# Optimization experiments

Hardware: AMD Instinct MI355X
Metric: run time of the kernel (lower is better)

## Reference

```python
import jax, jax.numpy as jnp
import numpy as np

B, N, D = 16, 256, 32


def setup_inputs() -> dict:
    key = jax.random.key(0)
    ks = jax.random.split(key, 9)
    s = lambda fan_in: 1.0 / np.sqrt(fan_in)
    return {
        "x": jax.random.normal(ks[0], (B, N, D), dtype=jnp.float32),
        # fc_out: Linear(2D -> D), stored as [in, out]
        "W_out": jax.random.uniform(ks[1], (2 * D, D), minval=-s(2 * D), maxval=s(2 * D)),
        "b_out": jax.random.uniform(ks[2], (D,), minval=-s(2 * D), maxval=s(2 * D)),
        # fc_cat: Linear(D -> 1)
        "W_cat": jax.random.uniform(ks[3], (D, 1), minval=-s(D), maxval=s(D)),
        "b_cat": jax.random.uniform(ks[4], (1,), minval=-s(D), maxval=s(D)),
        # att_fusion: Linear(2->8), ReLU, Linear(8->1), Sigmoid
        "W_f1": jax.random.uniform(ks[5], (2, 8), minval=-s(2), maxval=s(2)),
        "b_f1": jax.random.uniform(ks[6], (8,), minval=-s(2), maxval=s(2)),
        "W_f2": jax.random.uniform(ks[7], (8, 1), minval=-s(8), maxval=s(8)),
        "b_f2": jax.random.uniform(ks[8], (1,), minval=-s(8), maxval=s(8)),
    }


def reference(x, W_out, b_out, W_cat, b_cat, W_f1, b_f1, W_f2, b_f2):
    b, n, d = x.shape
    # Edge (i,j): receiver = x[:, i], sender = x[:, j] (off-diagonal only).
    # Vectorized over all N*N pairs instead of one-hot matmuls + batch loop.
    senders = jnp.broadcast_to(x[:, None, :, :], (b, n, n, d))    # x[j] at (i,j)
    receivers = jnp.broadcast_to(x[:, :, None, :], (b, n, n, d))  # x[i] at (i,j)
    pair = jnp.concatenate([senders, receivers], axis=-1)         # [B,N,N,2D]
    h = jax.nn.relu(pair @ W_out + b_out)                         # [B,N,N,D]
    e = jax.nn.relu(h @ W_cat + b_cat)                            # [B,N,N,1]
    off_diag = (1.0 - jnp.eye(n, dtype=x.dtype))[None, :, :, None]
    m_lin = e * off_diag                                          # zeros on diagonal (scatter equivalent)
    m_prod = jnp.einsum('bid,bjd->bij', x, x)[..., None]          # [B,N,N,1]
    fused = jnp.concatenate([m_lin, m_prod], axis=-1)             # [B,N,N,2]
    w = jax.nn.sigmoid(jax.nn.relu(fused @ W_f1 + b_f1) @ W_f2 + b_f2)  # [B,N,N,1]
    m = w * m_lin + (1.0 - w) * m_prod
    m = m + jnp.mean(m, axis=-2, keepdims=True)
    # F.layer_norm over shape[1:] = (N,N,1), no affine
    mu = jnp.mean(m, axis=(1, 2, 3), keepdims=True)
    var = jnp.var(m, axis=(1, 2, 3), keepdims=True)
    return (m - mu) / jnp.sqrt(var + 1e-5)
```

## Files before the change

### kernel.cpp

```cpp
#include <hip/hip_runtime.h>
#include <math.h>

#define BB 16
#define NN 256
#define DD 32

__global__ __launch_bounds__(256) void uvT_kernel(
    const float* __restrict__ x,
    const float* __restrict__ W_out,
    const float* __restrict__ b_out,
    float* __restrict__ uT, float* __restrict__ xT, float* __restrict__ vT)
{
    __shared__ float lxA[256];
    int t = threadIdx.x;
    int g0 = blockIdx.x * 8;
    lxA[t] = x[(size_t)g0 * DD + t];
    __syncthreads();

    int nl = t >> 5, d = t & 31;
    int b  = (g0 + nl) >> 8;
    int n  = (g0 + nl) & 255;
    float su = 0.f, sv = 0.f;
#pragma unroll
    for (int k = 0; k < DD; ++k) {
        float xv = lxA[nl * DD + k];
        su += xv * W_out[k * DD + d];
        sv += xv * W_out[(k + DD) * DD + d];
    }
    int idxT = ((b * 8 + (d >> 2)) * NN + n) * 4 + (d & 3);
    uT[idxT] = su;
    vT[idxT] = sv + b_out[d];
    xT[idxT] = lxA[nl * DD + d];
}

__global__ __launch_bounds__(256) void pair_kernel(
    const float* __restrict__ uT, const float* __restrict__ xT,
    const float* __restrict__ vT,
    const float* __restrict__ W_cat, const float* __restrict__ b_cat,
    const float* __restrict__ W_f1,  const float* __restrict__ b_f1,
    const float* __restrict__ W_f2,  const float* __restrict__ b_f2,
    float* __restrict__ m_out,
    float* __restrict__ rowsum_out, float* __restrict__ rowsq_out)
{
    __shared__ float red0[8][4], red1[8][4];

    const int t  = threadIdx.x;
    const int b  = blockIdx.x >> 5;
    const int i0 = (blockIdx.x & 31) * 8;

    const float4* uT4 = (const float4*)uT;
    const float4* xT4 = (const float4*)xT;
    const float4* vT4 = (const float4*)vT;

    float4 uj[8], xj[8];
#pragma unroll
    for (int q = 0; q < 8; ++q) {
        uj[q] = uT4[(b * 8 + q) * NN + t];
        xj[q] = xT4[(b * 8 + q) * NN + t];
    }

    const float4* Wc4 = (const float4*)W_cat;
    float4 wc[8];
#pragma unroll
    for (int q = 0; q < 8; ++q) wc[q] = Wc4[q];
    float f1a[8], f1b[8], fb1[8], f2w[8];
#pragma unroll
    for (int k = 0; k < 8; ++k) {
        f1a[k] = W_f1[k];
        f1b[k] = W_f1[8 + k];
        fb1[k] = b_f1[k];
        f2w[k] = W_f2[k];
    }
    const float bcat = b_cat[0], bf2 = b_f2[0];

    const int lane = t & 63, wv = t >> 6;
    float mreg[8];
#pragma unroll
    for (int r = 0; r < 8; ++r) {
        int i = i0 + r;
        float e = 0.f, mp = 0.f;
#pragma unroll
        for (int q = 0; q < 8; ++q) {
            float4 vi = vT4[(b * 8 + q) * NN + i];
            float4 xi = xT4[(b * 8 + q) * NN + i];
            float4 uu = uj[q], xx = xj[q];
            e += fmaxf(uu.x + vi.x, 0.f) * wc[q].x;
            e += fmaxf(uu.y + vi.y, 0.f) * wc[q].y;
            e += fmaxf(uu.z + vi.z, 0.f) * wc[q].z;
            e += fmaxf(uu.w + vi.w, 0.f) * wc[q].w;
            mp += xx.x * xi.x + xx.y * xi.y + xx.z * xi.z + xx.w * xi.w;
        }
        e = fmaxf(e + bcat, 0.f);
        float mlin = (t == i) ? 0.f : e;
        float s = bf2;
#pragma unroll
        for (int k = 0; k < 8; ++k)
            s += fmaxf(mlin * f1a[k] + mp * f1b[k] + fb1[k], 0.f) * f2w[k];
        float w = 1.f / (1.f + expf(-s));
        float m = w * mlin + (1.f - w) * mp;
        mreg[r] = m;

        float sm = m, sq = m * m;
#pragma unroll
        for (int off = 32; off; off >>= 1) {
            sm += __shfl_down(sm, off);
            sq += __shfl_down(sq, off);
        }
        if (lane == 0) { red0[r][wv] = sm; red1[r][wv] = sq; }
    }

#pragma unroll
    for (int r = 0; r < 8; ++r)
        m_out[((size_t)b * NN + i0 + r) * NN + t] = mreg[r];

    __syncthreads();
    if (t < 8) {
        rowsum_out[b * NN + i0 + t] = red0[t][0] + red0[t][1] + red0[t][2] + red0[t][3];
        rowsq_out [b * NN + i0 + t] = red1[t][0] + red1[t][1] + red1[t][2] + red1[t][3];
    }
}

__global__ __launch_bounds__(256) void final_kernel(
    const float* __restrict__ m_in,
    const float* __restrict__ rowsum, const float* __restrict__ rowsq,
    float* __restrict__ out)
{
    __shared__ float sred[12];
    __shared__ float stat[2];
    int t  = threadIdx.x;
    int b  = blockIdx.x >> 5;
    int r0 = (blockIdx.x & 31) * 8;

    float rs = rowsum[b * NN + t];
    float rq = rowsq [b * NN + t];
    float rr = rs * (1.f / NN);
    float sM = rs, sQ = rq, sR = rr * rr;
#pragma unroll
    for (int off = 32; off; off >>= 1) {
        sM += __shfl_down(sM, off);
        sQ += __shfl_down(sQ, off);
        sR += __shfl_down(sR, off);
    }
    int wave = t >> 6;
    if ((t & 63) == 0) { sred[wave] = sM; sred[4 + wave] = sQ; sred[8 + wave] = sR; }
    __syncthreads();
    if (t == 0) {
        float sumM  = sred[0] + sred[1] + sred[2] + sred[3];
        float sumQ  = sred[4] + sred[5] + sred[6] + sred[7];
        float sumR2 = sred[8] + sred[9] + sred[10] + sred[11];
        const float inv = 1.f / ((float)NN * (float)NN);
        float mu  = 2.f * sumM * inv;
        float ex2 = (sumQ + 3.f * (float)NN * sumR2) * inv;
        stat[0] = mu;
        stat[1] = rsqrtf(ex2 - mu * mu + 1e-5f);
    }
    __syncthreads();
    float mu = stat[0], rstd = stat[1];
#pragma unroll
    for (int r = 0; r < 8; ++r) {
        int i = r0 + r;
        size_t base = ((size_t)b * NN + i) * NN;
        float ri = rowsum[b * NN + i] * (1.f / NN);
        out[base + t] = (m_in[base + t] + ri - mu) * rstd;
    }
}

extern "C" void kernel_launch(void* const* d_in, const int* in_sizes, int n_in,
                              void* d_out, int out_size, void* d_ws, size_t ws_size,
                              hipStream_t stream)
{
    const float* x     = (const float*)d_in[0];
    const float* W_out = (const float*)d_in[1];
    const float* b_out = (const float*)d_in[2];
    const float* W_cat = (const float*)d_in[3];
    const float* b_cat = (const float*)d_in[4];
    const float* W_f1  = (const float*)d_in[5];
    const float* b_f1  = (const float*)d_in[6];
    const float* W_f2  = (const float*)d_in[7];
    const float* b_f2  = (const float*)d_in[8];

    float* ws     = (float*)d_ws;
    float* uT     = ws;
    float* xT     = uT + BB * NN * DD;
    float* vT     = xT + BB * NN * DD;
    float* m      = vT + BB * NN * DD;
    float* rowsum = m + (size_t)BB * NN * NN;
    float* rowsq  = rowsum + BB * NN;

    uvT_kernel <<<BB * NN / 8, 256, 0, stream>>>(x, W_out, b_out, uT, xT, vT);
    pair_kernel<<<BB * (NN / 8), 256, 0, stream>>>(uT, xT, vT, W_cat, b_cat,
                                                   W_f1, b_f1, W_f2, b_f2,
                                                   m, rowsum, rowsq);
    final_kernel<<<BB * (NN / 8), 256, 0, stream>>>(m, rowsum, rowsq, (float*)d_out);
}
```

Before: 25.42 us.

## Write pair results into output buffer in place, halve rows per block, use row-major v

Result: faster. 24.31 us (-4.4%).

```diff
diff --git a/kernel.cpp b/kernel.cpp
--- a/kernel.cpp
+++ b/kernel.cpp
@@ -4,12 +4,14 @@
 #define BB 16
 #define NN 256
 #define DD 32
+#define RG 4
+#define BPB (NN / RG)
 
 __global__ __launch_bounds__(256) void uvT_kernel(
     const float* __restrict__ x,
     const float* __restrict__ W_out,
     const float* __restrict__ b_out,
-    float* __restrict__ uT, float* __restrict__ xT, float* __restrict__ vT)
+    float* __restrict__ uT, float* __restrict__ xT, float* __restrict__ v)
 {
     __shared__ float lxA[256];
     int t = threadIdx.x;
@@ -29,28 +31,28 @@
     }
     int idxT = ((b * 8 + (d >> 2)) * NN + n) * 4 + (d & 3);
     uT[idxT] = su;
-    vT[idxT] = sv + b_out[d];
     xT[idxT] = lxA[nl * DD + d];
+    v[(size_t)(g0 + nl) * DD + d] = sv + b_out[d];
 }
 
 __global__ __launch_bounds__(256) void pair_kernel(
+    const float* __restrict__ x,
     const float* __restrict__ uT, const float* __restrict__ xT,
-    const float* __restrict__ vT,
+    const float* __restrict__ v,
     const float* __restrict__ W_cat, const float* __restrict__ b_cat,
     const float* __restrict__ W_f1,  const float* __restrict__ b_f1,
     const float* __restrict__ W_f2,  const float* __restrict__ b_f2,
-    float* __restrict__ m_out,
-    float* __restrict__ rowsum_out, float* __restrict__ rowsq_out)
+    float* __restrict__ rowsum, float* __restrict__ rowsq,
+    float* __restrict__ out)
 {
-    __shared__ float red0[8][4], red1[8][4];
+    __shared__ float red0[RG][4], red1[RG][4];
 
     const int t  = threadIdx.x;
-    const int b  = blockIdx.x >> 5;
-    const int i0 = (blockIdx.x & 31) * 8;
+    const int b  = blockIdx.x >> 6;
+    const int i0 = (blockIdx.x & 63) * RG;
 
     const float4* uT4 = (const float4*)uT;
     const float4* xT4 = (const float4*)xT;
-    const float4* vT4 = (const float4*)vT;
 
     float4 uj[8], xj[8];
 #pragma unroll
@@ -74,15 +76,16 @@
     const float bcat = b_cat[0], bf2 = b_f2[0];
 
     const int lane = t & 63, wv = t >> 6;
-    float mreg[8];
 #pragma unroll
-    for (int r = 0; r < 8; ++r) {
-        int i = i0 + r;
+    for (int r = 0; r < RG; ++r) {
+        const int i = i0 + r;
+        const float4* vrow = (const float4*)(v + ((size_t)b * NN + i) * DD);
+        const float4* xrow = (const float4*)(x + ((size_t)b * NN + i) * DD);
         float e = 0.f, mp = 0.f;
 #pragma unroll
         for (int q = 0; q < 8; ++q) {
-            float4 vi = vT4[(b * 8 + q) * NN + i];
-            float4 xi = xT4[(b * 8 + q) * NN + i];
+            float4 vi = vrow[q];
+            float4 xi = xrow[q];
             float4 uu = uj[q], xx = xj[q];
             e += fmaxf(uu.x + vi.x, 0.f) * wc[q].x;
             e += fmaxf(uu.y + vi.y, 0.f) * wc[q].y;
@@ -96,9 +99,10 @@
 #pragma unroll
         for (int k = 0; k < 8; ++k)
             s += fmaxf(mlin * f1a[k] + mp * f1b[k] + fb1[k], 0.f) * f2w[k];
-        float w = 1.f / (1.f + expf(-s));
+        float w = 1.f / (1.f + __expf(-s));
         float m = w * mlin + (1.f - w) * mp;
-        mreg[r] = m;
+
+        out[((size_t)b * NN + i) * NN + t] = m;
 
         float sm = m, sq = m * m;
 #pragma unroll
@@ -108,28 +112,22 @@
         }
         if (lane == 0) { red0[r][wv] = sm; red1[r][wv] = sq; }
     }
-
-#pragma unroll
-    for (int r = 0; r < 8; ++r)
-        m_out[((size_t)b * NN + i0 + r) * NN + t] = mreg[r];
-
     __syncthreads();
-    if (t < 8) {
-        rowsum_out[b * NN + i0 + t] = red0[t][0] + red0[t][1] + red0[t][2] + red0[t][3];
-        rowsq_out [b * NN + i0 + t] = red1[t][0] + red1[t][1] + red1[t][2] + red1[t][3];
+    if (t < RG) {
+        rowsum[b * NN + i0 + t] = red0[t][0] + red0[t][1] + red0[t][2] + red0[t][3];
+        rowsq [b * NN + i0 + t] = red1[t][0] + red1[t][1] + red1[t][2] + red1[t][3];
     }
 }
 
 __global__ __launch_bounds__(256) void final_kernel(
-    const float* __restrict__ m_in,
     const float* __restrict__ rowsum, const float* __restrict__ rowsq,
     float* __restrict__ out)
 {
     __shared__ float sred[12];
     __shared__ float stat[2];
-    int t  = threadIdx.x;
-    int b  = blockIdx.x >> 5;
-    int r0 = (blockIdx.x & 31) * 8;
+    const int t  = threadIdx.x;
+    const int b  = blockIdx.x >> 6;
+    const int i0 = (blockIdx.x & 63) * RG;
 
     float rs = rowsum[b * NN + t];
     float rq = rowsq [b * NN + t];
@@ -141,7 +139,7 @@
         sQ += __shfl_down(sQ, off);
         sR += __shfl_down(sR, off);
     }
-    int wave = t >> 6;
+    const int wave = t >> 6;
     if ((t & 63) == 0) { sred[wave] = sM; sred[4 + wave] = sQ; sred[8 + wave] = sR; }
     __syncthreads();
     if (t == 0) {
@@ -155,13 +153,13 @@
         stat[1] = rsqrtf(ex2 - mu * mu + 1e-5f);
     }
     __syncthreads();
-    float mu = stat[0], rstd = stat[1];
+    const float mu = stat[0], rstd = stat[1];
 #pragma unroll
-    for (int r = 0; r < 8; ++r) {
-        int i = r0 + r;
+    for (int r = 0; r < RG; ++r) {
+        int i = i0 + r;
         size_t base = ((size_t)b * NN + i) * NN;
         float ri = rowsum[b * NN + i] * (1.f / NN);
-        out[base + t] = (m_in[base + t] + ri - mu) * rstd;
+        out[base + t] = (out[base + t] + ri - mu) * rstd;
     }
 }
 
@@ -182,14 +180,14 @@
     float* ws     = (float*)d_ws;
     float* uT     = ws;
     float* xT     = uT + BB * NN * DD;
-    float* vT     = xT + BB * NN * DD;
-    float* m      = vT + BB * NN * DD;
-    float* rowsum = m + (size_t)BB * NN * NN;
+    float* v      = xT + BB * NN * DD;
+    float* rowsum = v + BB * NN * DD;
     float* rowsq  = rowsum + BB * NN;
+    float* outp   = (float*)d_out;
 
-    uvT_kernel <<<BB * NN / 8, 256, 0, stream>>>(x, W_out, b_out, uT, xT, vT);
-    pair_kernel<<<BB * (NN / 8), 256, 0, stream>>>(uT, xT, vT, W_cat, b_cat,
-                                                   W_f1, b_f1, W_f2, b_f2,
-                                                   m, rowsum, rowsq);
-    final_kernel<<<BB * (NN / 8), 256, 0, stream>>>(m, rowsum, rowsq, (float*)d_out);
+    uvT_kernel  <<<BB * NN / 8, 256, 0, stream>>>(x, W_out, b_out, uT, xT, v);
+    pair_kernel <<<BB * BPB, 256, 0, stream>>>(x, uT, xT, v, W_cat, b_cat,
+                                               W_f1, b_f1, W_f2, b_f2,
+                                               rowsum, rowsq, outp);
+    final_kernel<<<BB * BPB, 256, 0, stream>>>(rowsum, rowsq, outp);
 }
```
